# Performance work log

Hardware: AMD Instinct MI355X
Metric: run time of the kernel (lower is better)

## Reference

```python
import jax, jax.numpy as jnp
import numpy as np

NUM_SEQS = 8
SEQ_LEN = 2048
HIDDEN = 768
NUM_HEADS = 12
HEAD_DIM = 64
EPS = 1e-12


def setup_inputs() -> dict:
    key = jax.random.key(0)
    ks = jax.random.split(key, 12)
    total = NUM_SEQS * SEQ_LEN
    hidden_states = jax.random.normal(ks[0], (total, HIDDEN), dtype=jnp.float32)
    cu_seq_lens = jnp.arange(NUM_SEQS + 1, dtype=jnp.int32) * SEQ_LEN
    s = 0.02
    inp = {
        "hidden_states": hidden_states,
        "cu_seq_lens": cu_seq_lens,
        "max_seq_len": SEQ_LEN,
        "norm_w": jnp.ones((HIDDEN,), jnp.float32),
        "norm_b": jnp.zeros((HIDDEN,), jnp.float32),
        "Wq": jax.random.normal(ks[1], (HIDDEN, HIDDEN), jnp.float32) * s,
        "bq": jnp.zeros((HIDDEN,), jnp.float32),
        "Wk": jax.random.normal(ks[2], (HIDDEN, HIDDEN), jnp.float32) * s,
        "bk": jnp.zeros((HIDDEN,), jnp.float32),
        "Wv": jax.random.normal(ks[3], (HIDDEN, HIDDEN), jnp.float32) * s,
        "bv": jnp.zeros((HIDDEN,), jnp.float32),
        "Wo": jax.random.normal(ks[4], (HIDDEN, HIDDEN), jnp.float32) * s,
        "bo": jnp.zeros((HIDDEN,), jnp.float32),
    }
    return inp


def _layer_norm(x, w, b):
    mu = jnp.mean(x, axis=-1, keepdims=True)
    var = jnp.mean(jnp.square(x - mu), axis=-1, keepdims=True)
    return (x - mu) * jax.lax.rsqrt(var + EPS) * w + b


def _rope(x, positions, interleaved=False):
    # x: [t, h, d]; positions: [t]
    d = x.shape[-1]
    inv_freq = 1.0 / (10000.0 ** (jnp.arange(0, d, 2, dtype=jnp.float32) / d))  # [d/2]
    theta = positions.astype(jnp.float32)[:, None] * inv_freq[None, :]  # [t, d/2]
    cos = jnp.cos(theta)[:, None, :]  # [t, 1, d/2]
    sin = jnp.sin(theta)[:, None, :]
    x1, x2 = x[..., : d // 2], x[..., d // 2 :]
    return jnp.concatenate([x1 * cos - x2 * sin, x2 * cos + x1 * sin], axis=-1)


def _attention(q, k, v):
    # q,k,v: [b, s, h, d] (equal-length sequences, no padding)
    scale = 1.0 / jnp.sqrt(jnp.asarray(q.shape[-1], q.dtype))
    scores = jnp.einsum("bqhd,bkhd->bhqk", q, k) * scale
    probs = jax.nn.softmax(scores, axis=-1)
    return jnp.einsum("bhqk,bkhd->bqhd", probs, v)


def reference(hidden_states, cu_seq_lens, max_seq_len, norm_w, norm_b,
              Wq, bq, Wk, bk, Wv, bv, Wo, bo):
    t = hidden_states.shape[0]
    # pre_norm, layer_idx=1 -> LayerNorm
    x = _layer_norm(hidden_states, norm_w, norm_b)
    value = x @ Wv + bv
    query = x @ Wq + bq
    key = x @ Wk + bk

    def split(z):
        return z.reshape(t, NUM_HEADS, HEAD_DIM)

    q, k, v = split(query), split(key), split(value)

    # positions within each sequence (equal-length packing)
    positions = jnp.tile(jnp.arange(SEQ_LEN, dtype=jnp.int32), NUM_SEQS)
    q = _rope(q, positions)
    k = _rope(k, positions)

    # reshape packed -> [b, s, h, d]; sequences are equal-length here
    qb = q.reshape(NUM_SEQS, SEQ_LEN, NUM_HEADS, HEAD_DIM)
    kb = k.reshape(NUM_SEQS, SEQ_LEN, NUM_HEADS, HEAD_DIM)
    vb = v.reshape(NUM_SEQS, SEQ_LEN, NUM_HEADS, HEAD_DIM)
    attn = _attention(qb, kb, vb).reshape(t, HIDDEN)

    attn = attn @ Wo + bo
    # residual add (dropout prob = 0)
    out = attn + x
    return out
```

## Files before the change

kernel.cpp:

```cpp
#include <hip/hip_runtime.h>

typedef __bf16 bf16x8 __attribute__((ext_vector_type(8)));
typedef float  f32x4  __attribute__((ext_vector_type(4)));
typedef float  f32x16 __attribute__((ext_vector_type(16)));
typedef unsigned u32x2 __attribute__((ext_vector_type(2)));

#define MFMA16(a,b,c) __builtin_amdgcn_mfma_f32_16x16x32_bf16((a),(b),(c),0,0,0)
#define MFMA32(a,b,c) __builtin_amdgcn_mfma_f32_32x32x16_bf16((a),(b),(c),0,0,0)

constexpr int  HID  = 768;
constexpr long T    = 16384;
constexpr long SZ   = T * HID;
constexpr int  SEQ  = 2048;
constexpr int  NH   = 12;
constexpr int  HD   = 64;
constexpr int  WELE = HID * HID;

constexpr float QSCALE = 0.125f * 1.4426950408889634f;
constexpr float L10K32 = 13.287712379549449f / 32.0f;

__device__ __forceinline__ unsigned pkbf(float a, float b) {
    union { __bf16 h[2]; unsigned u; } x;
    x.h[0] = (__bf16)a; x.h[1] = (__bf16)b; return x.u;
}

__device__ __forceinline__ void gld16(const __bf16* g, __bf16* l) {
    __builtin_amdgcn_global_load_lds(
        (const __attribute__((address_space(1))) unsigned int*)g,
        (__attribute__((address_space(3))) unsigned int*)l, 16, 0, 0);
}

__global__ __launch_bounds__(256)
void wconv_kernel(const float* __restrict__ W0, __bf16* __restrict__ T0,
                  const float* __restrict__ W1, __bf16* __restrict__ T1,
                  const float* __restrict__ W2, __bf16* __restrict__ T2,
                  const float* __restrict__ W3, __bf16* __restrict__ T3) {
    const float* W; __bf16* Wt;
    switch (blockIdx.z) {
        case 0: W = W0; Wt = T0; break;
        case 1: W = W1; Wt = T1; break;
        case 2: W = W2; Wt = T2; break;
        default: W = W3; Wt = T3; break;
    }
    __shared__ float tile[64][65];
    int n0 = blockIdx.x * 64, k0 = blockIdx.y * 64;
    int c = threadIdx.x & 63, rr = threadIdx.x >> 6;
#pragma unroll
    for (int i = 0; i < 16; i++) {
        int r = i * 4 + rr;
        tile[r][c] = W[(long)(k0 + r) * HID + n0 + c];
    }
    __syncthreads();
#pragma unroll
    for (int i = 0; i < 16; i++) {
        int r = i * 4 + rr;
        Wt[(long)(n0 + r) * HID + k0 + c] = (__bf16)tile[c][r];
    }
}

__global__ __launch_bounds__(256)
void ln_kernel(const float* __restrict__ hs, const float* __restrict__ w,
               const float* __restrict__ b, __bf16* __restrict__ xbf) {
    int row = blockIdx.x, tid = threadIdx.x;
    const float* hr = hs + (long)row * HID;
    float v0 = hr[tid], v1 = hr[tid + 256], v2 = hr[tid + 512];
    float s  = v0 + v1 + v2;
    float s2 = v0 * v0 + v1 * v1 + v2 * v2;
#pragma unroll
    for (int off = 1; off < 64; off <<= 1) {
        s  += __shfl_xor(s, off);
        s2 += __shfl_xor(s2, off);
    }
    __shared__ float red[8];
    int wave = tid >> 6;
    if ((tid & 63) == 0) { red[wave] = s; red[4 + wave] = s2; }
    __syncthreads();
    s  = red[0] + red[1] + red[2] + red[3];
    s2 = red[4] + red[5] + red[6] + red[7];
    float mu   = s * (1.0f / HID);
    float var  = s2 * (1.0f / HID) - mu * mu;
    float rstd = rsqrtf(var + 1e-12f);
    long base = (long)row * HID;
    xbf[base + tid]       = (__bf16)((v0 - mu) * rstd * w[tid]       + b[tid]);
    xbf[base + tid + 256] = (__bf16)((v1 - mu) * rstd * w[tid + 256] + b[tid + 256]);
    xbf[base + tid + 512] = (__bf16)((v2 - mu) * rstd * w[tid + 512] + b[tid + 512]);
}

constexpr int SEGSZ = 528;

template <int MODE>
__global__ __launch_bounds__(256)
void gemm_lds(const __bf16* __restrict__ A, const __bf16* __restrict__ Bt,
              const float* __restrict__ bias, __bf16* __restrict__ outb,
              const __bf16* __restrict__ resid, float* __restrict__ outf,
              float scale) {
    int tid = threadIdx.x, wave = tid >> 6, lane = tid & 63;
    int lr = lane & 15, quad = lane >> 4;
    int wm = wave >> 1, wn = wave & 1;
    long m0 = (long)blockIdx.x * 128;
    int  n0 = blockIdx.y * 128;

    __shared__ __align__(16) __bf16 As[16 * SEGSZ];
    __shared__ __align__(16) __bf16 Bs[16 * SEGSZ];

    const f32x4 vzero = {0.f, 0.f, 0.f, 0.f};
    f32x4 acc[4][4];
#pragma unroll
    for (int ms = 0; ms < 4; ms++)
#pragma unroll
        for (int ns = 0; ns < 4; ns++) acc[ms][ns] = vzero;

    const __bf16* ga = A  + (long)(m0 + wave * 32 + (lane >> 3)) * HID + (lane & 7) * 8;
    const __bf16* gb = Bt + (long)(n0 + wave * 32 + (lane >> 3)) * HID + (lane & 7) * 8;
    __bf16* la = As + wave * 4 * SEGSZ;
    __bf16* lb = Bs + wave * 4 * SEGSZ;

    int fbase = (lr >> 3) * SEGSZ + (lr & 7) * 64 + quad * 8;

    for (int k0 = 0; k0 < HID; k0 += 64) {
#pragma unroll
        for (int j = 0; j < 4; j++) {
            gld16(ga + (long)j * 8 * HID + k0, la + j * SEGSZ);
            gld16(gb + (long)j * 8 * HID + k0, lb + j * SEGSZ);
        }
        __syncthreads();
#pragma unroll
        for (int kk = 0; kk < 64; kk += 32) {
            bf16x8 af[4], bfr[4];
#pragma unroll
            for (int ms = 0; ms < 4; ms++)
                af[ms] = *(const bf16x8*)&As[fbase + (wm * 8 + ms * 2) * SEGSZ + kk];
#pragma unroll
            for (int ns = 0; ns < 4; ns++)
                bfr[ns] = *(const bf16x8*)&Bs[fbase + (wn * 8 + ns * 2) * SEGSZ + kk];
#pragma unroll
            for (int ms = 0; ms < 4; ms++)
#pragma unroll
                for (int ns = 0; ns < 4; ns++)
                    acc[ms][ns] = MFMA16(af[ms], bfr[ns], acc[ms][ns]);
        }
        __syncthreads();
    }

    if (MODE == 1) {
#pragma unroll
        for (int ms = 0; ms < 4; ms++)
#pragma unroll
        for (int r = 0; r < 4; r++) {
            int d = (int)(m0 + wm * 64 + ms * 16 + quad * 4 + r);
            float bv = bias[d];
            int hh = d >> 6, dd = d & 63;
#pragma unroll
            for (int ns = 0; ns < 4; ns++) {
                int posg = n0 + wn * 64 + ns * 16 + lr;
                int sq = posg >> 11, pos = posg & (SEQ - 1);
                outb[((long)((sq * NH + hh) * HD + dd) << 11) + pos] =
                    (__bf16)(acc[ms][ns][r] + bv);
            }
        }
    } else {
#pragma unroll
        for (int ns = 0; ns < 4; ns++) {
            int col = n0 + wn * 64 + ns * 16 + lr;
            float bv = bias[col];
#pragma unroll
            for (int ms = 0; ms < 4; ms++)
#pragma unroll
            for (int r = 0; r < 4; r++) {
                long row = m0 + wm * 64 + ms * 16 + quad * 4 + r;
                outf[row * HID + col] = acc[ms][ns][r] + bv + (float)resid[row * HID + col];
            }
        }
    }
}

__global__ __launch_bounds__(256, 2)
void gemm_qk(const __bf16* __restrict__ A, const __bf16* __restrict__ Btq,
             const __bf16* __restrict__ Btk,
             const float* __restrict__ biasq, const float* __restrict__ biask,
             __bf16* __restrict__ outq, __bf16* __restrict__ outk) {
    int tid = threadIdx.x, wave = tid >> 6, lane = tid & 63;
    int lr = lane & 15, quad = lane >> 4;
    int wm = wave >> 1, wn = wave & 1;
    long m0 = (long)blockIdx.x * 128;
    int  n0 = blockIdx.y * 128;

    __shared__ __align__(16) __bf16 As[16 * SEGSZ];
    __shared__ __align__(16) __bf16 Bqs[16 * SEGSZ];
    __shared__ __align__(16) __bf16 Bks[16 * SEGSZ];

    const f32x4 vzero = {0.f, 0.f, 0.f, 0.f};
    f32x4 accq[4][4], acck[4][4];
#pragma unroll
    for (int ms = 0; ms < 4; ms++)
#pragma unroll
        for (int ns = 0; ns < 4; ns++) { accq[ms][ns] = vzero; acck[ms][ns] = vzero; }

    const __bf16* ga = A   + (long)(m0 + wave * 32 + (lane >> 3)) * HID + (lane & 7) * 8;
    const __bf16* gq = Btq + (long)(n0 + wave * 32 + (lane >> 3)) * HID + (lane & 7) * 8;
    const __bf16* gk = Btk + (long)(n0 + wave * 32 + (lane >> 3)) * HID + (lane & 7) * 8;
    __bf16* la = As  + wave * 4 * SEGSZ;
    __bf16* lq = Bqs + wave * 4 * SEGSZ;
    __bf16* lk = Bks + wave * 4 * SEGSZ;

    int fbase = (lr >> 3) * SEGSZ + (lr & 7) * 64 + quad * 8;

    for (int k0 = 0; k0 < HID; k0 += 64) {
#pragma unroll
        for (int j = 0; j < 4; j++) {
            gld16(ga + (long)j * 8 * HID + k0, la + j * SEGSZ);
            gld16(gq + (long)j * 8 * HID + k0, lq + j * SEGSZ);
            gld16(gk + (long)j * 8 * HID + k0, lk + j * SEGSZ);
        }
        __syncthreads();
#pragma unroll
        for (int kk = 0; kk < 64; kk += 32) {
            bf16x8 af[4], bqf[4], bkf[4];
#pragma unroll
            for (int ms = 0; ms < 4; ms++)
                af[ms] = *(const bf16x8*)&As[fbase + (wm * 8 + ms * 2) * SEGSZ + kk];
#pragma unroll
            for (int ns = 0; ns < 4; ns++) {
                bqf[ns] = *(const bf16x8*)&Bqs[fbase + (wn * 8 + ns * 2) * SEGSZ + kk];
                bkf[ns] = *(const bf16x8*)&Bks[fbase + (wn * 8 + ns * 2) * SEGSZ + kk];
            }
#pragma unroll
            for (int ms = 0; ms < 4; ms++)
#pragma unroll
                for (int ns = 0; ns < 4; ns++) {
                    accq[ms][ns] = MFMA16(af[ms], bqf[ns], accq[ms][ns]);
                    acck[ms][ns] = MFMA16(af[ms], bkf[ns], acck[ms][ns]);
                }
        }
        __syncthreads();
    }

    int hb = n0 + wn * 64;
    float f1 = __builtin_amdgcn_exp2f(-(float)lr * L10K32);
    float f2 = __builtin_amdgcn_exp2f(-(float)(lr + 16) * L10K32);
    {
        float b0 = biasq[hb + lr],      b1 = biasq[hb + 16 + lr];
        float b2 = biasq[hb + 32 + lr], b3 = biasq[hb + 48 + lr];
#pragma unroll
        for (int ms = 0; ms < 4; ms++)
#pragma unroll
        for (int r = 0; r < 4; r++) {
            long row = m0 + wm * 64 + ms * 16 + quad * 4 + r;
            int pos = (int)(row & (SEQ - 1));
            float s1, c1, s2, c2;
            __sincosf((float)pos * f1, &s1, &c1);
            __sincosf((float)pos * f2, &s2, &c2);
            float v0 = accq[ms][0][r] + b0, v1 = accq[ms][1][r] + b1;
            float v2 = accq[ms][2][r] + b2, v3 = accq[ms][3][r] + b3;
            __bf16* ob = outq + row * HID + hb;
            ob[lr]      = (__bf16)((v0 * c1 - v2 * s1) * QSCALE);
            ob[16 + lr] = (__bf16)((v1 * c2 - v3 * s2) * QSCALE);
            ob[32 + lr] = (__bf16)((v2 * c1 + v0 * s1) * QSCALE);
            ob[48 + lr] = (__bf16)((v3 * c2 + v1 * s2) * QSCALE);
        }
    }
    {
        float b0 = biask[hb + lr],      b1 = biask[hb + 16 + lr];
        float b2 = biask[hb + 32 + lr], b3 = biask[hb + 48 + lr];
#pragma unroll
        for (int ms = 0; ms < 4; ms++)
#pragma unroll
        for (int r = 0; r < 4; r++) {
            long row = m0 + wm * 64 + ms * 16 + quad * 4 + r;
            int pos = (int)(row & (SEQ - 1));
            float s1, c1, s2, c2;
            __sincosf((float)pos * f1, &s1, &c1);
            __sincosf((float)pos * f2, &s2, &c2);
            float v0 = acck[ms][0][r] + b0, v1 = acck[ms][1][r] + b1;
            float v2 = acck[ms][2][r] + b2, v3 = acck[ms][3][r] + b3;
            __bf16* ob = outk + row * HID + hb;
            ob[lr]      = (__bf16)(v0 * c1 - v2 * s1);
            ob[16 + lr] = (__bf16)(v1 * c2 - v3 * s2);
            ob[32 + lr] = (__bf16)(v2 * c1 + v0 * s1);
            ob[48 + lr] = (__bf16)(v3 * c2 + v1 * s2);
        }
    }
}

__global__ __launch_bounds__(256)
void attn_kernel(const __bf16* __restrict__ q, const __bf16* __restrict__ k,
                 const __bf16* __restrict__ vt, __bf16* __restrict__ att) {
    int tid = threadIdx.x, wave = tid >> 6, lane = tid & 63;
    int c = lane & 31, hi = lane >> 5;
    int bb = blockIdx.x;
    int s  = bb & 7;
    int ii = bb >> 3;
    int h  = ii >> 4;
    int qt = ii & 15;
    long q0 = (long)s * SEQ + qt * 128 + wave * 32;

    __shared__ __align__(16) __bf16 Ks[2][64 * 64];
    __shared__ __align__(16) __bf16 Vs[2][64 * 64];

    bf16x8 qf[4];
    {
        const __bf16* qrow = q + (q0 + c) * HID + h * HD + hi * 8;
#pragma unroll
        for (int kk = 0; kk < 4; kk++)
            qf[kk] = *(const bf16x8*)(qrow + kk * 16);
    }

    const __bf16 onebf = (__bf16)1.0f;
    const bf16x8 ones = {onebf, onebf, onebf, onebf, onebf, onebf, onebf, onebf};

    f32x16 o[2] = {};
    f32x16 lsx = {};

    const __bf16* kg = k  + (long)s * SEQ * HID + h * HD;
    const __bf16* vg = vt + (long)(s * NH + h) * HD * SEQ;

    int srow = lane >> 3;
    int sgch = (lane & 7) ^ srow;

#define STAGE(bufi, kv)                                                         \
    {                                                                           \
        _Pragma("unroll")                                                       \
        for (int rr = 0; rr < 2; rr++) {                                        \
            int grp = rr * 4 + wave;                                            \
            gld16(kg + (long)((kv) + grp * 8 + srow) * HID + sgch * 8,          \
                  &Ks[bufi][(grp * 8) * 64]);                                   \
            gld16(vg + (long)(grp * 8 + srow) * SEQ + (kv) + sgch * 8,          \
                  &Vs[bufi][(grp * 8) * 64]);                                   \
        }                                                                       \
    }

#define ATTN_BODY(BUF)                                                          \
    {                                                                           \
        f32x16 st0 = {}, st1 = {};                                              \
        __builtin_amdgcn_s_setprio(1);                                          \
        _Pragma("unroll")                                                       \
        for (int kk = 0; kk < 4; kk++) {                                        \
            bf16x8 kf0 = *(const bf16x8*)                                       \
                &Ks[BUF][c * 64 + ((((kk << 1) + hi) ^ (c & 7)) << 3)];         \
            st0 = MFMA32(kf0, qf[kk], st0);                                     \
            bf16x8 kf1 = *(const bf16x8*)                                       \
                &Ks[BUF][(32 + c) * 64 + ((((kk << 1) + hi) ^ (c & 7)) << 3)];  \
            st1 = MFMA32(kf1, qf[kk], st1);                                     \
        }                                                                       \
        __builtin_amdgcn_s_setprio(0);                                          \
        bf16x8 pb[4];                                                           \
        _Pragma("unroll")                                                       \
        for (int kh = 0; kh < 2; kh++) {                                        \
            unsigned pk[8];                                                     \
            _Pragma("unroll")                                                   \
            for (int i = 0; i < 8; i++) {                                       \
                float e0 = __builtin_amdgcn_exp2f(kh ? st1[2 * i] : st0[2 * i]);        \
                float e1 = __builtin_amdgcn_exp2f(kh ? st1[2 * i + 1] : st0[2 * i + 1]);\
                pk[i] = pkbf(e0, e1);                                           \
            }                                                                   \
            _Pragma("unroll")                                                   \
            for (int b = 0; b < 2; b++) {                                       \
                u32x2 r02 = __builtin_amdgcn_permlane32_swap(                   \
                    pk[4 * b + 0], pk[4 * b + 2], false, false);                \
                u32x2 r13 = __builtin_amdgcn_permlane32_swap(                   \
                    pk[4 * b + 1], pk[4 * b + 3], false, false);                \
                union { unsigned u[4]; bf16x8 v; } pu;                          \
                pu.u[0] = r02[0]; pu.u[1] = r13[0];                             \
                pu.u[2] = r02[1]; pu.u[3] = r13[1];                             \
                pb[2 * kh + b] = pu.v;                                          \
            }                                                                   \
        }                                                                       \
        __builtin_amdgcn_s_setprio(1);                                          \
        _Pragma("unroll")                                                       \
        for (int kk = 0; kk < 4; kk++) {                                        \
            lsx = MFMA32(ones, pb[kk], lsx);                                    \
            bf16x8 vf0 = *(const bf16x8*)                                       \
                &Vs[BUF][c * 64 + ((((kk << 1) + hi) ^ (c & 7)) << 3)];         \
            o[0] = MFMA32(vf0, pb[kk], o[0]);                                   \
            bf16x8 vf1 = *(const bf16x8*)                                       \
                &Vs[BUF][(32 + c) * 64 + ((((kk << 1) + hi) ^ (c & 7)) << 3)];  \
            o[1] = MFMA32(vf1, pb[kk], o[1]);                                   \
        }                                                                       \
        __builtin_amdgcn_s_setprio(0);                                          \
    }

#define WAITV(N) asm volatile("s_waitcnt vmcnt(" #N ")" ::: "memory")
#define BAR()    asm volatile("s_barrier" ::: "memory")

    STAGE(0, 0)
    STAGE(1, 64)

#pragma unroll 1
    for (int t2 = 0; t2 < 15; t2++) {
        WAITV(4);
        BAR();
        ATTN_BODY(0)
        BAR();
        STAGE(0, (2 * t2 + 2) * 64)
        WAITV(4);
        BAR();
        ATTN_BODY(1)
        BAR();
        STAGE(1, (2 * t2 + 3) * 64)
    }
    WAITV(4);
    BAR();
    ATTN_BODY(0)
    WAITV(0);
    BAR();
    ATTN_BODY(1)

#undef WAITV
#undef BAR
#undef STAGE
#undef ATTN_BODY

    float inv = 1.0f / lsx[0];
    __bf16* ob = att + (q0 + c) * HID + h * HD;
#pragma unroll
    for (int dh = 0; dh < 2; dh++)
#pragma unroll
        for (int a = 0; a < 4; a++) {
            unsigned lo  = pkbf(o[dh][4 * a] * inv,     o[dh][4 * a + 1] * inv);
            unsigned hi2 = pkbf(o[dh][4 * a + 2] * inv, o[dh][4 * a + 3] * inv);
            int d = dh * 32 + a * 8 + hi * 4;
            *(unsigned long long*)&ob[d] =
                ((unsigned long long)hi2 << 32) | lo;
        }
}

extern "C" void kernel_launch(void* const* d_in, const int* in_sizes, int n_in,
                              void* d_out, int out_size, void* d_ws, size_t ws_size,
                              hipStream_t stream) {
    const float* hs    = (const float*)d_in[0];
    const float* normw = (const float*)d_in[3];
    const float* normb = (const float*)d_in[4];
    const float* Wq = (const float*)d_in[5];
    const float* bq = (const float*)d_in[6];
    const float* Wk = (const float*)d_in[7];
    const float* bk = (const float*)d_in[8];
    const float* Wv = (const float*)d_in[9];
    const float* bv = (const float*)d_in[10];
    const float* Wo = (const float*)d_in[11];
    const float* bo = (const float*)d_in[12];

    __bf16* base = (__bf16*)d_ws;
    __bf16* x   = base;
    __bf16* qb  = base + SZ;
    __bf16* kb  = base + 2 * SZ;
    __bf16* vtb = base + 3 * SZ;
    __bf16* att = base + 4 * SZ;
    __bf16* wqt = base + 5 * SZ;
    __bf16* wkt = wqt + WELE;
    __bf16* wvt = wkt + WELE;
    __bf16* wot = wvt + WELE;

    wconv_kernel<<<dim3(12, 12, 4), 256, 0, stream>>>(Wq, wqt, Wk, wkt, Wv, wvt, Wo, wot);

    ln_kernel<<<(int)T, 256, 0, stream>>>(hs, normw, normb, x);

    gemm_qk<<<dim3(T / 128, HID / 128), 256, 0, stream>>>(x, wqt, wkt, bq, bk, qb, kb);
    gemm_lds<1><<<dim3(HID / 128, T / 128), 256, 0, stream>>>(wvt, x, bv, vtb, nullptr, nullptr, 1.0f);

    attn_kernel<<<dim3(NH * 16 * 8), 256, 0, stream>>>(qb, kb, vtb, att);

    gemm_lds<2><<<dim3(T / 128, HID / 128), 256, 0, stream>>>(att, wot, bo, nullptr, x, (float*)d_out, 1.0f);
}
```

Before: 399.6 us.

## Enlarge attention blocks to 8 waves, triple-buffer KV, sum softmax on VALU

The attention kernel now runs 512-thread blocks covering 256 query rows each, so every K/V tile staged into LDS is shared by twice as many waves. The LDS ring grows from double to triple buffering, which removes one barrier per tile and issues the next load before the current tile is computed. The row-sum MFMA against a vector of ones is replaced by a scalar VALU accumulation plus a cross-half shuffle at the end. The trade-offs are more LDS per block, fewer blocks in the grid, and extra VALU adds in the exp loop.

After: 405.8 us. Within noise of the previous version (+1.6%).

```diff
diff --git a/kernel.cpp b/kernel.cpp
--- a/kernel.cpp
+++ b/kernel.cpp
@@ -282,7 +282,7 @@
     }
 }
 
-__global__ __launch_bounds__(256)
+__global__ __launch_bounds__(512)
 void attn_kernel(const __bf16* __restrict__ q, const __bf16* __restrict__ k,
                  const __bf16* __restrict__ vt, __bf16* __restrict__ att) {
     int tid = threadIdx.x, wave = tid >> 6, lane = tid & 63;
@@ -290,12 +290,12 @@
     int bb = blockIdx.x;
     int s  = bb & 7;
     int ii = bb >> 3;
-    int h  = ii >> 4;
-    int qt = ii & 15;
-    long q0 = (long)s * SEQ + qt * 128 + wave * 32;
-
-    __shared__ __align__(16) __bf16 Ks[2][64 * 64];
-    __shared__ __align__(16) __bf16 Vs[2][64 * 64];
+    int h  = ii >> 3;
+    int qt = ii & 7;
+    long q0 = (long)s * SEQ + qt * 256 + wave * 32;
+
+    __shared__ __align__(16) __bf16 Ks[3][64 * 64];
+    __shared__ __align__(16) __bf16 Vs[3][64 * 64];
 
     bf16x8 qf[4];
     {
@@ -305,11 +305,8 @@
             qf[kk] = *(const bf16x8*)(qrow + kk * 16);
     }
 
-    const __bf16 onebf = (__bf16)1.0f;
-    const bf16x8 ones = {onebf, onebf, onebf, onebf, onebf, onebf, onebf, onebf};
-
     f32x16 o[2] = {};
-    f32x16 lsx = {};
+    float ls = 0.f;
 
     const __bf16* kg = k  + (long)s * SEQ * HID + h * HD;
     const __bf16* vg = vt + (long)(s * NH + h) * HD * SEQ;
@@ -319,14 +316,10 @@
 
 #define STAGE(bufi, kv)                                                         \
     {                                                                           \
-        _Pragma("unroll")                                                       \
-        for (int rr = 0; rr < 2; rr++) {                                        \
-            int grp = rr * 4 + wave;                                            \
-            gld16(kg + (long)((kv) + grp * 8 + srow) * HID + sgch * 8,          \
-                  &Ks[bufi][(grp * 8) * 64]);                                   \
-            gld16(vg + (long)(grp * 8 + srow) * SEQ + (kv) + sgch * 8,          \
-                  &Vs[bufi][(grp * 8) * 64]);                                   \
-        }                                                                       \
+        gld16(kg + (long)((kv) + wave * 8 + srow) * HID + sgch * 8,             \
+              &Ks[bufi][(wave * 8) * 64]);                                      \
+        gld16(vg + (long)(wave * 8 + srow) * SEQ + (kv) + sgch * 8,             \
+              &Vs[bufi][(wave * 8) * 64]);                                      \
     }
 
 #define ATTN_BODY(BUF)                                                          \
@@ -351,6 +344,7 @@
             for (int i = 0; i < 8; i++) {                                       \
                 float e0 = __builtin_amdgcn_exp2f(kh ? st1[2 * i] : st0[2 * i]);        \
                 float e1 = __builtin_amdgcn_exp2f(kh ? st1[2 * i + 1] : st0[2 * i + 1]);\
+                ls += e0 + e1;                                                  \
                 pk[i] = pkbf(e0, e1);                                           \
             }                                                                   \
             _Pragma("unroll")                                                   \
@@ -368,7 +362,6 @@
         __builtin_amdgcn_s_setprio(1);                                          \
         _Pragma("unroll")                                                       \
         for (int kk = 0; kk < 4; kk++) {                                        \
-            lsx = MFMA32(ones, pb[kk], lsx);                                    \
             bf16x8 vf0 = *(const bf16x8*)                                       \
                 &Vs[BUF][c * 64 + ((((kk << 1) + hi) ^ (c & 7)) << 3)];         \
             o[0] = MFMA32(vf0, pb[kk], o[0]);                                   \
@@ -386,23 +379,21 @@
     STAGE(1, 64)
 
 #pragma unroll 1
-    for (int t2 = 0; t2 < 15; t2++) {
-        WAITV(4);
-        BAR();
+    for (int u = 0; u < 10; u++) {
+        int kv = u * 3 * 64;
+        WAITV(2); BAR();
+        STAGE(2, kv + 2 * 64)
         ATTN_BODY(0)
-        BAR();
-        STAGE(0, (2 * t2 + 2) * 64)
-        WAITV(4);
-        BAR();
+        WAITV(2); BAR();
+        STAGE(0, kv + 3 * 64)
         ATTN_BODY(1)
-        BAR();
-        STAGE(1, (2 * t2 + 3) * 64)
-    }
-    WAITV(4);
-    BAR();
+        WAITV(2); BAR();
+        STAGE(1, kv + 4 * 64)
+        ATTN_BODY(2)
+    }
+    WAITV(2); BAR();
     ATTN_BODY(0)
-    WAITV(0);
-    BAR();
+    WAITV(0); BAR();
     ATTN_BODY(1)
 
 #undef WAITV
@@ -410,7 +401,8 @@
 #undef STAGE
 #undef ATTN_BODY
 
-    float inv = 1.0f / lsx[0];
+    ls += __shfl_xor(ls, 32);
+    float inv = 1.0f / ls;
     __bf16* ob = att + (q0 + c) * HID + h * HD;
 #pragma unroll
     for (int dh = 0; dh < 2; dh++)
@@ -457,7 +449,7 @@
     gemm_qk<<<dim3(T / 128, HID / 128), 256, 0, stream>>>(x, wqt, wkt, bq, bk, qb, kb);
     gemm_lds<1><<<dim3(HID / 128, T / 128), 256, 0, stream>>>(wvt, x, bv, vtb, nullptr, nullptr, 1.0f);
 
-    attn_kernel<<<dim3(NH * 16 * 8), 256, 0, stream>>>(qb, kb, vtb, att);
+    attn_kernel<<<dim3(NH * 8 * 8), 512, 0, stream>>>(qb, kb, vtb, att);
 
     gemm_lds<2><<<dim3(T / 128, HID / 128), 256, 0, stream>>>(att, wot, bo, nullptr, x, (float*)d_out, 1.0f);
 }
```
